# Kernel optimization log

Measured on AMD Instinct MI355X. Metric: run time of the kernel, lower is better.

## Reference

```python
import jax, jax.numpy as jnp
import numpy as np
import math

N_HEAD = 16


def _causal_attn(q, k, v):
    # q: [B,H,L,d], k/v: [B,H,S,d]; standard scaled-dot-product causal attention
    d_k = q.shape[-1]
    s = jnp.einsum('bhqd,bhkd->bhqk', q, k) / math.sqrt(d_k)
    L, S = q.shape[-2], k.shape[-2]
    mask = jnp.tril(jnp.ones((L, S), dtype=bool))
    s = jnp.where(mask, s, -jnp.inf)
    a = jax.nn.softmax(s, axis=-1)
    return jnp.einsum('bhqk,bhkd->bhqd', a, v)


def setup_inputs() -> dict:
    key = jax.random.key(0)
    ks = jax.random.split(key, 8)
    B, T, C = 2, 2048, 1024
    scale = 0.02
    return {
        'x': jax.random.normal(ks[0], (B, T, C), dtype=jnp.float32),
        'W_attn': jax.random.normal(ks[1], (C, 2 * C), dtype=jnp.float32) * scale,
        'b_attn': jnp.zeros((2 * C,), dtype=jnp.float32),
        'W_k2': jax.random.normal(ks[2], (C, C), dtype=jnp.float32) * scale,
        'b_k2': jnp.zeros((C,), dtype=jnp.float32),
        'W_proj': jax.random.normal(ks[3], (C, C), dtype=jnp.float32) * scale,
        'b_proj': jnp.zeros((C,), dtype=jnp.float32),
    }


def reference(x, W_attn, b_attn, W_k2, b_k2, W_proj, b_proj):
    # Eval-mode forward of CausalSelfAttentionARMA (all dropouts inactive).
    B, T, C = x.shape
    H = N_HEAD
    d = C // H

    qk = x @ W_attn + b_attn                      # [B,T,2C]
    q, k = qk[..., :C], qk[..., C:]
    q = q.reshape(B, T, H, d).transpose(0, 2, 1, 3)   # [B,H,T,d]
    k = k.reshape(B, T, H, d).transpose(0, 2, 1, 3)
    v = x.reshape(B, T, H, d).transpose(0, 2, 1, 3)   # v = x (no value proj)

    # AR pass: standard causal attention
    y = _causal_attn(q, k, v)                     # [B,H,T,d]

    # MA residual: e_t = v_{t+1} - y_t
    e = v[:, :, 1:, :] - y[:, :, :-1, :]          # [B,H,T-1,d]

    k2 = (x[:, :-1] @ W_k2 + b_k2).reshape(B, T - 1, H, d).transpose(0, 2, 1, 3)
    q2 = q[:, :, 1:, :]

    # MA pass: second causal attention over residuals
    y2 = _causal_attn(q2, k2, e)                  # [B,H,T-1,d]
    y2 = jnp.concatenate([jnp.zeros_like(y2[:, :, :1, :]), y2], axis=2)  # [B,H,T,d]

    def proj(t):
        return t.transpose(0, 2, 1, 3).reshape(B, T, C) @ W_proj + b_proj

    return proj(y) + proj(y2)
```

## Files before the change

kernel.cpp:

```cpp
#include <hip/hip_runtime.h>
#include <hip/hip_bf16.h>

typedef unsigned short u16;
typedef short s16x8 __attribute__((ext_vector_type(8)));
typedef float f32x4 __attribute__((ext_vector_type(4)));
typedef float f32x16 __attribute__((ext_vector_type(16)));
typedef unsigned int u32x4 __attribute__((ext_vector_type(4)));

#define LOG2E 1.44269504088896f

__device__ __forceinline__ u16 f2b(float f){
    __hip_bfloat16 h = __float2bfloat16(f);
    return __builtin_bit_cast(unsigned short, h);
}
__device__ __forceinline__ float b2f(u16 u){
    __hip_bfloat16 h = __builtin_bit_cast(__hip_bfloat16, u);
    return __bfloat162float(h);
}
__device__ __forceinline__ unsigned int pk2(float a, float b){
    return (unsigned int)f2b(a) | ((unsigned int)f2b(b) << 16);
}
__device__ __forceinline__ unsigned int cvtpk(float lo, float hi){
    unsigned int r;
    asm("v_cvt_pk_bf16_f32 %0, %1, %2" : "=v"(r) : "v"(lo), "v"(hi));
    return r;
}

__global__ void k_f32_to_bf16(const float* __restrict__ in, u16* __restrict__ out, int n4){
    int i = blockIdx.x*blockDim.x + threadIdx.x;
    int stride = gridDim.x*blockDim.x;
    for (; i < n4; i += stride){
        float4 a = *(const float4*)&in[(size_t)i*4];
        uint2 o;
        o.x = pk2(a.x, a.y);
        o.y = pk2(a.z, a.w);
        *(uint2*)&out[(size_t)i*4] = o;
    }
}

__global__ void k_transpose_bf16(const float* __restrict__ W, u16* __restrict__ Wt, int K, int N){
    __shared__ float tile[32][33];
    int n0 = blockIdx.x*32, k0 = blockIdx.y*32;
    int c = threadIdx.x & 31, r0 = threadIdx.x >> 5;
#pragma unroll
    for (int it = 0; it < 4; ++it){
        int r = r0 + it*8;
        tile[r][c] = W[(size_t)(k0+r)*N + n0 + c];
    }
    __syncthreads();
#pragma unroll
    for (int it = 0; it < 4; ++it){
        int r = r0 + it*8;
        Wt[(size_t)(n0+r)*K + k0 + c] = f2b(tile[c][r]);
    }
}

__global__ __launch_bounds__(256) void k_build_vT(const float* __restrict__ x, u16* __restrict__ VT){
    __shared__ float tile[64][65];
    int bh = blockIdx.x, t0 = blockIdx.y*64;
    int b = bh >> 4, h = bh & 15;
    int tid = threadIdx.x;
    {
        int tt = tid >> 2, ds = (tid & 3)*16;
        const float* xp = &x[((size_t)(b*2048) + t0 + tt)*1024 + h*64 + ds];
#pragma unroll
        for (int j4 = 0; j4 < 4; ++j4){
            float4 a = *(const float4*)&xp[j4*4];
            tile[tt][ds + j4*4 + 0] = a.x;
            tile[tt][ds + j4*4 + 1] = a.y;
            tile[tt][ds + j4*4 + 2] = a.z;
            tile[tt][ds + j4*4 + 3] = a.w;
        }
    }
    __syncthreads();
    {
        int dd = tid >> 2, ts = (tid & 3)*16;
        unsigned int o[8];
#pragma unroll
        for (int j = 0; j < 8; ++j)
            o[j] = pk2(tile[ts + 2*j][dd], tile[ts + 2*j + 1][dd]);
        u16* dst = &VT[((size_t)(bh*64 + dd))*2048 + t0 + ts];
        *(uint4*)&dst[0] = *(uint4*)&o[0];
        *(uint4*)&dst[8] = *(uint4*)&o[4];
    }
}

__global__ __launch_bounds__(256) void k_compute_eT(const float* __restrict__ x, const float* __restrict__ y1T,
                                                    u16* __restrict__ ET){
    __shared__ float tile[64][65];
    int bh = blockIdx.x, j0 = blockIdx.y*64;
    int b = bh >> 4, h = bh & 15;
    int tid = threadIdx.x;
    {
        int tt = tid >> 2, ds = (tid & 3)*16;
        int j = j0 + tt;
        int xr = (j <= 2046) ? (j + 1) : 2047;
        const float* xp = &x[((size_t)(b*2048) + xr)*1024 + h*64 + ds];
#pragma unroll
        for (int j4 = 0; j4 < 4; ++j4){
            float4 a = *(const float4*)&xp[j4*4];
            tile[tt][ds + j4*4 + 0] = a.x;
            tile[tt][ds + j4*4 + 1] = a.y;
            tile[tt][ds + j4*4 + 2] = a.z;
            tile[tt][ds + j4*4 + 3] = a.w;
        }
    }
    __syncthreads();
    {
        int dd = tid >> 2, ts = (tid & 3)*16;
        const float* yp = &y1T[((size_t)(bh*64 + dd))*2048 + j0 + ts];
        unsigned int o[8];
#pragma unroll
        for (int j = 0; j < 8; ++j){
            int c0 = ts + 2*j, c1 = ts + 2*j + 1;
            float e0 = (j0 + c0 <= 2046) ? (tile[c0][dd] - yp[2*j])   : 0.f;
            float e1 = (j0 + c1 <= 2046) ? (tile[c1][dd] - yp[2*j+1]) : 0.f;
            o[j] = pk2(e0, e1);
        }
        u16* dst = &ET[((size_t)(bh*64 + dd))*2048 + j0 + ts];
        *(uint4*)&dst[0] = *(uint4*)&o[0];
        *(uint4*)&dst[8] = *(uint4*)&o[4];
    }
}

template<int MODE>
__global__ __launch_bounds__(256) void k_gemm(const u16* __restrict__ A, const u16* __restrict__ Bt,
                       const float* __restrict__ bias, float* __restrict__ outF,
                       u16* __restrict__ out0, u16* __restrict__ out1,
                       int M, int N, int K){
    __shared__ u16 As[128][72];
    __shared__ u16 Bs[128][72];
    int m0 = blockIdx.y * 128, n0 = blockIdx.x * 128;
    int tid = threadIdx.x;
    int lane = tid & 63, w = tid >> 6;
    int wm = w >> 1, wn = w & 1;
    int l15 = lane & 15, l4 = lane >> 4;
    f32x4 acc[4][4] = {};

    for (int kt = 0; kt < K; kt += 64){
#pragma unroll
        for (int it = 0; it < 4; ++it){
            int c = tid + 256*it;
            int row = c >> 3, seg = c & 7;
            *(uint4*)&As[row][seg*8] = *(const uint4*)&A[(size_t)(m0+row)*K + kt + seg*8];
            *(uint4*)&Bs[row][seg*8] = *(const uint4*)&Bt[(size_t)(n0+row)*K + kt + seg*8];
        }
        __syncthreads();
#pragma unroll
        for (int kk = 0; kk < 2; ++kk){
            s16x8 a[4], b[4];
#pragma unroll
            for (int mi = 0; mi < 4; ++mi)
                a[mi] = *(const s16x8*)&As[wm*64 + mi*16 + l15][kk*32 + l4*8];
#pragma unroll
            for (int ni = 0; ni < 4; ++ni)
                b[ni] = *(const s16x8*)&Bs[wn*64 + ni*16 + l15][kk*32 + l4*8];
#pragma unroll
            for (int mi = 0; mi < 4; ++mi)
#pragma unroll
                for (int ni = 0; ni < 4; ++ni)
                    acc[mi][ni] = __builtin_amdgcn_mfma_f32_16x16x32_bf16(a[mi], b[ni], acc[mi][ni], 0,0,0);
        }
        __syncthreads();
    }

#pragma unroll
    for (int mi = 0; mi < 4; ++mi){
        int growb = m0 + wm*64 + mi*16 + l4*4;
#pragma unroll
        for (int ni = 0; ni < 4; ++ni){
            int gcol = n0 + wn*64 + ni*16 + l15;
            float bv = bias[gcol];
#pragma unroll
            for (int r = 0; r < 4; ++r){
                int row = growb + r;
                float val = acc[mi][ni][r];
                if (MODE == 2){
                    outF[(size_t)row*N + gcol] = val + 2.0f*bv;
                } else {
                    val += bv;
                    int bb = row >> 11, t = row & 2047;
                    if (MODE == 0){
                        if (gcol < 1024){
                            int h = gcol >> 6, dd = gcol & 63;
                            out0[(((size_t)(bb*16+h))*2048 + t)*64 + dd] = f2b(val*0.125f);
                        } else {
                            int c2 = gcol - 1024;
                            int h = c2 >> 6, dd = c2 & 63;
                            out1[(((size_t)(bb*16+h))*2048 + t)*64 + dd] = f2b(val);
                        }
                    } else {
                        int h = gcol >> 6, dd = gcol & 63;
                        out0[(((size_t)(bb*16+h))*2048 + t)*64 + dd] = f2b(val);
                    }
                }
            }
        }
    }
}

__global__ __launch_bounds__(128) void k_flashw(const u16* __restrict__ Q, const u16* __restrict__ Km,
                         const u16* __restrict__ VT, float* __restrict__ OT,
                         int Tq, int qoff){
    int bh = blockIdx.x;
    int y = blockIdx.y;
    int t = (y < 16) ? (15 - (y >> 1)) : ((y - 16) >> 1);
    int half = y & 1;
    int tid = threadIdx.x;
    int w = tid >> 6, lane = tid & 63;
    int l31 = lane & 31, hi = lane >> 5;
    const u16* Qp = Q + ((size_t)bh*2048 + qoff)*64;
    const u16* Kp = Km + (size_t)bh*2048*64;
    const u16* Vp = VT + (size_t)bh*64*2048;
    float* Op = OT + (size_t)bh*64*2048;

    int q0w = t*128 + half*64 + w*32;
    int qi = q0w + l31; if (qi > Tq-1) qi = Tq-1;
    int nt = (q0w >> 6) + 1;

    s16x8 qf[4];
#pragma unroll
    for (int st = 0; st < 4; ++st)
        qf[st] = *(const s16x8*)&Qp[(size_t)qi*64 + st*16 + hi*8];

    f32x16 accO[2] = {};
    float m_r = -INFINITY, l_r = 0.f;

    for (int i = 0; i < nt; ++i){
        int kv0 = i*64;
        const u16* kb = Kp + (size_t)kv0*64;
        f32x16 s0 = {}, s1 = {};
        {
            const u16* kr0 = kb + (size_t)l31*64 + hi*8;
            const u16* kr1 = kb + (size_t)(32 + l31)*64 + hi*8;
            s16x8 a0 = *(const s16x8*)&kr0[0];
            s16x8 a1 = *(const s16x8*)&kr0[16];
            s16x8 a2 = *(const s16x8*)&kr0[32];
            s16x8 a3 = *(const s16x8*)&kr0[48];
            s16x8 b0 = *(const s16x8*)&kr1[0];
            s16x8 b1 = *(const s16x8*)&kr1[16];
            s16x8 b2 = *(const s16x8*)&kr1[32];
            s16x8 b3 = *(const s16x8*)&kr1[48];
            __builtin_amdgcn_s_setprio(1);
            s0 = __builtin_amdgcn_mfma_f32_32x32x16_bf16(a0, qf[0], s0, 0,0,0);
            s1 = __builtin_amdgcn_mfma_f32_32x32x16_bf16(b0, qf[0], s1, 0,0,0);
            s0 = __builtin_amdgcn_mfma_f32_32x32x16_bf16(a1, qf[1], s0, 0,0,0);
            s1 = __builtin_amdgcn_mfma_f32_32x32x16_bf16(b1, qf[1], s1, 0,0,0);
            s0 = __builtin_amdgcn_mfma_f32_32x32x16_bf16(a2, qf[2], s0, 0,0,0);
            s1 = __builtin_amdgcn_mfma_f32_32x32x16_bf16(b2, qf[2], s1, 0,0,0);
            s0 = __builtin_amdgcn_mfma_f32_32x32x16_bf16(a3, qf[3], s0, 0,0,0);
            s1 = __builtin_amdgcn_mfma_f32_32x32x16_bf16(b3, qf[3], s1, 0,0,0);
            __builtin_amdgcn_s_setprio(0);
        }
        if (i == nt - 1){
#pragma unroll
            for (int r = 0; r < 16; ++r){
                int kg0 = kv0 + (r&3) + 8*(r>>2) + 4*hi;
                if (kg0 > qi) s0[r] = -INFINITY;
                if (kg0 + 32 > qi) s1[r] = -INFINITY;
            }
        }
        float mx = s0[0];
#pragma unroll
        for (int r = 1; r < 16; ++r) mx = fmaxf(mx, s0[r]);
#pragma unroll
        for (int r = 0; r < 16; ++r) mx = fmaxf(mx, s1[r]);
        mx = fmaxf(mx, __shfl_xor(mx, 32));
        float mnew = fmaxf(m_r, mx);
        if (!__all(mx - m_r <= 8.f)){
            float scl = exp2f((m_r - mnew)*LOG2E);
#pragma unroll
            for (int dt = 0; dt < 2; ++dt)
#pragma unroll
                for (int r = 0; r < 16; ++r) accO[dt][r] *= scl;
            l_r *= scl;
            m_r = mnew;
        }
        float bl = m_r * LOG2E;
        float rs = 0.f;
#pragma unroll
        for (int r = 0; r < 16; ++r){
            s0[r] = exp2f(__builtin_fmaf(s0[r], LOG2E, -bl));
            rs += s0[r];
        }
#pragma unroll
        for (int r = 0; r < 16; ++r){
            s1[r] = exp2f(__builtin_fmaf(s1[r], LOG2E, -bl));
            rs += s1[r];
        }
        rs += __shfl_xor(rs, 32);
        l_r += rs;
#pragma unroll
        for (int g = 0; g < 4; ++g){
            int off = (g & 1)*8;
            unsigned dwa, dwb, dwc, dwd;
            if (g < 2){
                dwa = cvtpk(s0[off+0], s0[off+1]);
                dwb = cvtpk(s0[off+2], s0[off+3]);
                dwc = cvtpk(s0[off+4], s0[off+5]);
                dwd = cvtpk(s0[off+6], s0[off+7]);
            } else {
                dwa = cvtpk(s1[off+0], s1[off+1]);
                dwb = cvtpk(s1[off+2], s1[off+3]);
                dwc = cvtpk(s1[off+4], s1[off+5]);
                dwd = cvtpk(s1[off+6], s1[off+7]);
            }
            unsigned xa = (unsigned)__shfl_xor((int)dwa, 32);
            unsigned xb = (unsigned)__shfl_xor((int)dwb, 32);
            unsigned xc = (unsigned)__shfl_xor((int)dwc, 32);
            unsigned xd = (unsigned)__shfl_xor((int)dwd, 32);
            u32x4 fv;
            fv.x = hi ? xc : dwa;
            fv.y = hi ? xd : dwb;
            fv.z = hi ? dwc : xa;
            fv.w = hi ? dwd : xb;
            s16x8 pf = __builtin_bit_cast(s16x8, fv);
            int vslot = g*2 + hi;
            s16x8 va0 = *(const s16x8*)&Vp[(size_t)l31*2048 + kv0 + vslot*8];
            s16x8 va1 = *(const s16x8*)&Vp[(size_t)(32 + l31)*2048 + kv0 + vslot*8];
            __builtin_amdgcn_s_setprio(1);
            accO[0] = __builtin_amdgcn_mfma_f32_32x32x16_bf16(va0, pf, accO[0], 0,0,0);
            accO[1] = __builtin_amdgcn_mfma_f32_32x32x16_bf16(va1, pf, accO[1], 0,0,0);
            __builtin_amdgcn_s_setprio(0);
        }
    }
    float inv = 1.0f / l_r;
#pragma unroll
    for (int dt = 0; dt < 2; ++dt)
#pragma unroll
        for (int r = 0; r < 16; ++r){
            int d = dt*32 + (r&3) + 8*(r>>2) + 4*hi;
            Op[(size_t)d*2048 + qi] = accO[dt][r] * inv;
        }
}

__global__ __launch_bounds__(256) void k_ysum(const float* __restrict__ y1T, const float* __restrict__ y2T,
                                              u16* __restrict__ ys){
    __shared__ float tile[64][65];
    int bh = blockIdx.x, t0 = blockIdx.y*64;
    int b = bh >> 4, h = bh & 15;
    int tid = threadIdx.x;
    {
        int dd = tid >> 2, ts = (tid & 3)*16;
        const float* y1p = &y1T[((size_t)(bh*64 + dd))*2048 + t0 + ts];
        const float* y2p = &y2T[((size_t)(bh*64 + dd))*2048 + t0 + ts - 1];
#pragma unroll
        for (int c = 0; c < 16; ++c){
            int tg = t0 + ts + c;
            float s = y1p[c];
            if (tg > 0) s += y2p[c];
            tile[ts + c][dd] = s;
        }
    }
    __syncthreads();
    {
        int tt = tid >> 2, ds = (tid & 3)*16;
        unsigned int o[8];
#pragma unroll
        for (int j = 0; j < 8; ++j)
            o[j] = pk2(tile[tt][ds + 2*j], tile[tt][ds + 2*j + 1]);
        u16* dst = &ys[((size_t)(b*2048) + t0 + tt)*1024 + h*64 + ds];
        *(uint4*)&dst[0] = *(uint4*)&o[0];
        *(uint4*)&dst[8] = *(uint4*)&o[4];
    }
}

extern "C" void kernel_launch(void* const* d_in, const int* in_sizes, int n_in,
                              void* d_out, int out_size, void* d_ws, size_t ws_size,
                              hipStream_t stream){
    const float* x      = (const float*)d_in[0];
    const float* W_attn = (const float*)d_in[1];
    const float* b_attn = (const float*)d_in[2];
    const float* W_k2   = (const float*)d_in[3];
    const float* b_k2   = (const float*)d_in[4];
    const float* W_proj = (const float*)d_in[5];
    const float* b_proj = (const float*)d_in[6];
    float* out = (float*)d_out;

    char* ws = (char*)d_ws;
    size_t off = 0;
    auto alloc = [&](size_t bytes)->void*{
        void* p = ws + off; off += (bytes + 255) & ~size_t(255); return p;
    };
    u16* xb    = (u16*)alloc((size_t)4096*1024*2);
    u16* WaT   = (u16*)alloc((size_t)2048*1024*2);
    u16* Wk2T  = (u16*)alloc((size_t)1024*1024*2);
    u16* WpT   = (u16*)alloc((size_t)1024*1024*2);
    u16* Qb    = (u16*)alloc((size_t)32*2048*64*2);
    u16* Kb    = (u16*)alloc((size_t)32*2048*64*2);
    u16* VTg   = (u16*)alloc((size_t)32*64*2048*2);
    u16* K2b   = (u16*)alloc((size_t)32*2048*64*2);
    u16* ETg   = (u16*)alloc((size_t)32*64*2048*2);
    float* y1T = (float*)alloc((size_t)32*64*2048*4);
    float* y2T = (float*)alloc((size_t)32*64*2048*4);
    u16* ys    = (u16*)alloc((size_t)4096*1024*2);

    k_f32_to_bf16<<<1024, 256, 0, stream>>>(x, xb, 1<<20);
    k_transpose_bf16<<<dim3(64, 32), 256, 0, stream>>>(W_attn, WaT, 1024, 2048);
    k_transpose_bf16<<<dim3(32, 32), 256, 0, stream>>>(W_k2, Wk2T, 1024, 1024);
    k_transpose_bf16<<<dim3(32, 32), 256, 0, stream>>>(W_proj, WpT, 1024, 1024);
    k_build_vT<<<dim3(32, 32), 256, 0, stream>>>(x, VTg);

    k_gemm<0><<<dim3(16, 32), 256, 0, stream>>>(xb, WaT, b_attn, nullptr, Qb, Kb, 4096, 2048, 1024);
    k_gemm<1><<<dim3(8, 32), 256, 0, stream>>>(xb, Wk2T, b_k2, nullptr, K2b, nullptr, 4096, 1024, 1024);

    k_flashw<<<dim3(32, 32), 128, 0, stream>>>(Qb, Kb, VTg, y1T, 2048, 0);
    k_compute_eT<<<dim3(32, 32), 256, 0, stream>>>(x, y1T, ETg);
    k_flashw<<<dim3(32, 32), 128, 0, stream>>>(Qb, K2b, ETg, y2T, 2047, 1);
    k_ysum<<<dim3(32, 32), 256, 0, stream>>>(y1T, y2T, ys);

    k_gemm<2><<<dim3(8, 32), 256, 0, stream>>>(ys, WpT, b_proj, out, nullptr, nullptr, 4096, 1024, 1024);
}
```

Baseline: 363.5 us.

## Double-buffer K fragments and prefetch V in flash attention loop

Restructures the flash-attention inner loop so the next tile's K fragments load into a ping-pong register buffer while the current tile's softmax and PV run. All V fragments for the tile are now loaded at the start of the step instead of just before each PV MFMA. The row max and sum reductions become tree reductions, and the cross-half shuffle now moves 2 dwords per group instead of 4. This is meant to hide global load latency and shorten dependency chains, at the cost of more live registers, which may lower occupancy or cause spills.

```diff
diff --git a/kernel.cpp b/kernel.cpp
--- a/kernel.cpp
+++ b/kernel.cpp
@@ -12,10 +12,6 @@
 __device__ __forceinline__ u16 f2b(float f){
     __hip_bfloat16 h = __float2bfloat16(f);
     return __builtin_bit_cast(unsigned short, h);
-}
-__device__ __forceinline__ float b2f(u16 u){
-    __hip_bfloat16 h = __builtin_bit_cast(__hip_bfloat16, u);
-    return __bfloat162float(h);
 }
 __device__ __forceinline__ unsigned int pk2(float a, float b){
     return (unsigned int)f2b(a) | ((unsigned int)f2b(b) << 16);
@@ -199,6 +195,108 @@
     }
 }
 
+#define LOADK(dst, kvoff) do { \
+    const u16* kr0_ = Kp + (size_t)(kvoff)*64 + (size_t)l31*64 + hi*8; \
+    const u16* kr1_ = Kp + (size_t)(kvoff)*64 + (size_t)(32+l31)*64 + hi*8; \
+    dst[0] = *(const s16x8*)&kr0_[0];  dst[1] = *(const s16x8*)&kr0_[16]; \
+    dst[2] = *(const s16x8*)&kr0_[32]; dst[3] = *(const s16x8*)&kr0_[48]; \
+    dst[4] = *(const s16x8*)&kr1_[0];  dst[5] = *(const s16x8*)&kr1_[16]; \
+    dst[6] = *(const s16x8*)&kr1_[32]; dst[7] = *(const s16x8*)&kr1_[48]; \
+} while(0)
+
+#define FLASH_STEP(KC, KN) do { \
+    int kv0 = i*64; \
+    s16x8 w0[4], w1[4]; \
+    { const u16* vb_ = Vp + kv0; \
+      w0[0] = *(const s16x8*)&vb_[(size_t)l31*2048 + (0*2+hi)*8]; \
+      w1[0] = *(const s16x8*)&vb_[(size_t)(32+l31)*2048 + (0*2+hi)*8]; \
+      w0[1] = *(const s16x8*)&vb_[(size_t)l31*2048 + (1*2+hi)*8]; \
+      w1[1] = *(const s16x8*)&vb_[(size_t)(32+l31)*2048 + (1*2+hi)*8]; \
+      w0[2] = *(const s16x8*)&vb_[(size_t)l31*2048 + (2*2+hi)*8]; \
+      w1[2] = *(const s16x8*)&vb_[(size_t)(32+l31)*2048 + (2*2+hi)*8]; \
+      w0[3] = *(const s16x8*)&vb_[(size_t)l31*2048 + (3*2+hi)*8]; \
+      w1[3] = *(const s16x8*)&vb_[(size_t)(32+l31)*2048 + (3*2+hi)*8]; } \
+    f32x16 s0 = {}, s1 = {}; \
+    __builtin_amdgcn_s_setprio(1); \
+    s0 = __builtin_amdgcn_mfma_f32_32x32x16_bf16(KC[0], qf[0], s0, 0,0,0); \
+    s1 = __builtin_amdgcn_mfma_f32_32x32x16_bf16(KC[4], qf[0], s1, 0,0,0); \
+    s0 = __builtin_amdgcn_mfma_f32_32x32x16_bf16(KC[1], qf[1], s0, 0,0,0); \
+    s1 = __builtin_amdgcn_mfma_f32_32x32x16_bf16(KC[5], qf[1], s1, 0,0,0); \
+    s0 = __builtin_amdgcn_mfma_f32_32x32x16_bf16(KC[2], qf[2], s0, 0,0,0); \
+    s1 = __builtin_amdgcn_mfma_f32_32x32x16_bf16(KC[6], qf[2], s1, 0,0,0); \
+    s0 = __builtin_amdgcn_mfma_f32_32x32x16_bf16(KC[3], qf[3], s0, 0,0,0); \
+    s1 = __builtin_amdgcn_mfma_f32_32x32x16_bf16(KC[7], qf[3], s1, 0,0,0); \
+    __builtin_amdgcn_s_setprio(0); \
+    if (i + 1 < nt) LOADK(KN, kv0 + 64); \
+    if (i == nt - 1){ \
+        _Pragma("unroll") \
+        for (int r = 0; r < 16; ++r){ \
+            int kg0 = kv0 + (r&3) + 8*(r>>2) + 4*hi; \
+            if (kg0 > qi) s0[r] = -INFINITY; \
+            if (kg0 + 32 > qi) s1[r] = -INFINITY; \
+        } \
+    } \
+    float tm[16]; \
+    _Pragma("unroll") \
+    for (int r = 0; r < 16; ++r) tm[r] = fmaxf(s0[r], s1[r]); \
+    _Pragma("unroll") \
+    for (int r = 0; r < 8; ++r) tm[r] = fmaxf(tm[r], tm[r+8]); \
+    _Pragma("unroll") \
+    for (int r = 0; r < 4; ++r) tm[r] = fmaxf(tm[r], tm[r+4]); \
+    tm[0] = fmaxf(fmaxf(tm[0], tm[2]), fmaxf(tm[1], tm[3])); \
+    float mx = fmaxf(tm[0], __shfl_xor(tm[0], 32)); \
+    float mnew = fmaxf(m_r, mx); \
+    if (!__all(mx - m_r <= 8.f)){ \
+        float scl = exp2f((m_r - mnew)*LOG2E); \
+        _Pragma("unroll") \
+        for (int r = 0; r < 16; ++r) accO[0][r] *= scl; \
+        _Pragma("unroll") \
+        for (int r = 0; r < 16; ++r) accO[1][r] *= scl; \
+        l_r *= scl; \
+        m_r = mnew; \
+    } \
+    float bl = m_r * LOG2E; \
+    _Pragma("unroll") \
+    for (int r = 0; r < 16; ++r) s0[r] = exp2f(__builtin_fmaf(s0[r], LOG2E, -bl)); \
+    _Pragma("unroll") \
+    for (int r = 0; r < 16; ++r) s1[r] = exp2f(__builtin_fmaf(s1[r], LOG2E, -bl)); \
+    float ts[16]; \
+    _Pragma("unroll") \
+    for (int r = 0; r < 16; ++r) ts[r] = s0[r] + s1[r]; \
+    _Pragma("unroll") \
+    for (int r = 0; r < 8; ++r) ts[r] += ts[r+8]; \
+    _Pragma("unroll") \
+    for (int r = 0; r < 4; ++r) ts[r] += ts[r+4]; \
+    ts[0] = (ts[0] + ts[2]) + (ts[1] + ts[3]); \
+    l_r += ts[0] + __shfl_xor(ts[0], 32); \
+    _Pragma("unroll") \
+    for (int g = 0; g < 4; ++g){ \
+        unsigned dwa, dwb, dwc, dwd; \
+        if (g == 0){ dwa = cvtpk(s0[0], s0[1]); dwb = cvtpk(s0[2], s0[3]); \
+                     dwc = cvtpk(s0[4], s0[5]); dwd = cvtpk(s0[6], s0[7]); } \
+        else if (g == 1){ dwa = cvtpk(s0[8], s0[9]);  dwb = cvtpk(s0[10], s0[11]); \
+                          dwc = cvtpk(s0[12], s0[13]); dwd = cvtpk(s0[14], s0[15]); } \
+        else if (g == 2){ dwa = cvtpk(s1[0], s1[1]); dwb = cvtpk(s1[2], s1[3]); \
+                          dwc = cvtpk(s1[4], s1[5]); dwd = cvtpk(s1[6], s1[7]); } \
+        else { dwa = cvtpk(s1[8], s1[9]);  dwb = cvtpk(s1[10], s1[11]); \
+               dwc = cvtpk(s1[12], s1[13]); dwd = cvtpk(s1[14], s1[15]); } \
+        unsigned su = hi ? dwa : dwc; \
+        unsigned sv = hi ? dwb : dwd; \
+        unsigned pu = (unsigned)__shfl_xor((int)su, 32); \
+        unsigned pv = (unsigned)__shfl_xor((int)sv, 32); \
+        u32x4 fv; \
+        fv.x = hi ? pu : dwa; \
+        fv.y = hi ? pv : dwb; \
+        fv.z = hi ? dwc : pu; \
+        fv.w = hi ? dwd : pv; \
+        s16x8 pf = __builtin_bit_cast(s16x8, fv); \
+        __builtin_amdgcn_s_setprio(1); \
+        accO[0] = __builtin_amdgcn_mfma_f32_32x32x16_bf16(w0[g], pf, accO[0], 0,0,0); \
+        accO[1] = __builtin_amdgcn_mfma_f32_32x32x16_bf16(w1[g], pf, accO[1], 0,0,0); \
+        __builtin_amdgcn_s_setprio(0); \
+    } \
+} while(0)
+
 __global__ __launch_bounds__(128) void k_flashw(const u16* __restrict__ Q, const u16* __restrict__ Km,
                          const u16* __restrict__ VT, float* __restrict__ OT,
                          int Tq, int qoff){
@@ -226,104 +324,16 @@
     f32x16 accO[2] = {};
     float m_r = -INFINITY, l_r = 0.f;
 
-    for (int i = 0; i < nt; ++i){
-        int kv0 = i*64;
-        const u16* kb = Kp + (size_t)kv0*64;
-        f32x16 s0 = {}, s1 = {};
-        {
-            const u16* kr0 = kb + (size_t)l31*64 + hi*8;
-            const u16* kr1 = kb + (size_t)(32 + l31)*64 + hi*8;
-            s16x8 a0 = *(const s16x8*)&kr0[0];
-            s16x8 a1 = *(const s16x8*)&kr0[16];
-            s16x8 a2 = *(const s16x8*)&kr0[32];
-            s16x8 a3 = *(const s16x8*)&kr0[48];
-            s16x8 b0 = *(const s16x8*)&kr1[0];
-            s16x8 b1 = *(const s16x8*)&kr1[16];
-            s16x8 b2 = *(const s16x8*)&kr1[32];
-            s16x8 b3 = *(const s16x8*)&kr1[48];
-            __builtin_amdgcn_s_setprio(1);
-            s0 = __builtin_amdgcn_mfma_f32_32x32x16_bf16(a0, qf[0], s0, 0,0,0);
-            s1 = __builtin_amdgcn_mfma_f32_32x32x16_bf16(b0, qf[0], s1, 0,0,0);
-            s0 = __builtin_amdgcn_mfma_f32_32x32x16_bf16(a1, qf[1], s0, 0,0,0);
-            s1 = __builtin_amdgcn_mfma_f32_32x32x16_bf16(b1, qf[1], s1, 0,0,0);
-            s0 = __builtin_amdgcn_mfma_f32_32x32x16_bf16(a2, qf[2], s0, 0,0,0);
-            s1 = __builtin_amdgcn_mfma_f32_32x32x16_bf16(b2, qf[2], s1, 0,0,0);
-            s0 = __builtin_amdgcn_mfma_f32_32x32x16_bf16(a3, qf[3], s0, 0,0,0);
-            s1 = __builtin_amdgcn_mfma_f32_32x32x16_bf16(b3, qf[3], s1, 0,0,0);
-            __builtin_amdgcn_s_setprio(0);
-        }
-        if (i == nt - 1){
-#pragma unroll
-            for (int r = 0; r < 16; ++r){
-                int kg0 = kv0 + (r&3) + 8*(r>>2) + 4*hi;
-                if (kg0 > qi) s0[r] = -INFINITY;
-                if (kg0 + 32 > qi) s1[r] = -INFINITY;
-            }
-        }
-        float mx = s0[0];
-#pragma unroll
-        for (int r = 1; r < 16; ++r) mx = fmaxf(mx, s0[r]);
-#pragma unroll
-        for (int r = 0; r < 16; ++r) mx = fmaxf(mx, s1[r]);
-        mx = fmaxf(mx, __shfl_xor(mx, 32));
-        float mnew = fmaxf(m_r, mx);
-        if (!__all(mx - m_r <= 8.f)){
-            float scl = exp2f((m_r - mnew)*LOG2E);
-#pragma unroll
-            for (int dt = 0; dt < 2; ++dt)
-#pragma unroll
-                for (int r = 0; r < 16; ++r) accO[dt][r] *= scl;
-            l_r *= scl;
-            m_r = mnew;
-        }
-        float bl = m_r * LOG2E;
-        float rs = 0.f;
-#pragma unroll
-        for (int r = 0; r < 16; ++r){
-            s0[r] = exp2f(__builtin_fmaf(s0[r], LOG2E, -bl));
-            rs += s0[r];
-        }
-#pragma unroll
-        for (int r = 0; r < 16; ++r){
-            s1[r] = exp2f(__builtin_fmaf(s1[r], LOG2E, -bl));
-            rs += s1[r];
-        }
-        rs += __shfl_xor(rs, 32);
-        l_r += rs;
-#pragma unroll
-        for (int g = 0; g < 4; ++g){
-            int off = (g & 1)*8;
-            unsigned dwa, dwb, dwc, dwd;
-            if (g < 2){
-                dwa = cvtpk(s0[off+0], s0[off+1]);
-                dwb = cvtpk(s0[off+2], s0[off+3]);
-                dwc = cvtpk(s0[off+4], s0[off+5]);
-                dwd = cvtpk(s0[off+6], s0[off+7]);
-            } else {
-                dwa = cvtpk(s1[off+0], s1[off+1]);
-                dwb = cvtpk(s1[off+2], s1[off+3]);
-                dwc = cvtpk(s1[off+4], s1[off+5]);
-                dwd = cvtpk(s1[off+6], s1[off+7]);
-            }
-            unsigned xa = (unsigned)__shfl_xor((int)dwa, 32);
-            unsigned xb = (unsigned)__shfl_xor((int)dwb, 32);
-            unsigned xc = (unsigned)__shfl_xor((int)dwc, 32);
-            unsigned xd = (unsigned)__shfl_xor((int)dwd, 32);
-            u32x4 fv;
-            fv.x = hi ? xc : dwa;
-            fv.y = hi ? xd : dwb;
-            fv.z = hi ? dwc : xa;
-            fv.w = hi ? dwd : xb;
-            s16x8 pf = __builtin_bit_cast(s16x8, fv);
-            int vslot = g*2 + hi;
-            s16x8 va0 = *(const s16x8*)&Vp[(size_t)l31*2048 + kv0 + vslot*8];
-            s16x8 va1 = *(const s16x8*)&Vp[(size_t)(32 + l31)*2048 + kv0 + vslot*8];
-            __builtin_amdgcn_s_setprio(1);
-            accO[0] = __builtin_amdgcn_mfma_f32_32x32x16_bf16(va0, pf, accO[0], 0,0,0);
-            accO[1] = __builtin_amdgcn_mfma_f32_32x32x16_bf16(va1, pf, accO[1], 0,0,0);
-            __builtin_amdgcn_s_setprio(0);
-        }
-    }
+    s16x8 kA[8], kB[8];
+    LOADK(kA, 0);
+    int i = 0;
+    while (true){
+        FLASH_STEP(kA, kB);
+        ++i; if (i >= nt) break;
+        FLASH_STEP(kB, kA);
+        ++i; if (i >= nt) break;
+    }
+
     float inv = 1.0f / l_r;
 #pragma unroll
     for (int dt = 0; dt < 2; ++dt)
```

Measured after the change: 363.4 us. Within noise of the previous version (-0.0%).
